# Kernel optimization log

Hardware: AMD Instinct MI355X
Metric: run time of the kernel (lower is better)

Reference implementation:

```python
import jax, jax.numpy as jnp
import numpy as np

N = 100000      # n_nodes
E = 1600000     # n_edges (avg degree 16)
F_IN = 128      # data.num_features
HID = 16        # hidden dim from ChebConv(F_IN, 16, K=2)
K = 2


def setup_inputs() -> dict:
    key = jax.random.key(0)
    k0, k1, k2, k3 = jax.random.split(key, 4)
    x = jax.random.normal(k0, (N, F_IN), dtype=jnp.float32)
    edge_index = jax.random.randint(k1, (2, E), 0, N, dtype=jnp.int64)
    W1 = jax.random.normal(k2, (K, F_IN, HID), dtype=jnp.float32) / np.float32(np.sqrt(F_IN))
    b1 = jnp.zeros((HID,), jnp.float32)
    W2 = jax.random.normal(k3, (K, HID, F_IN), dtype=jnp.float32) / np.float32(np.sqrt(HID))
    b2 = jnp.zeros((F_IN,), jnp.float32)
    return {"x": x, "edge_index": edge_index, "W1": W1, "b1": b1, "W2": W2, "b2": b2}


def _cheb_conv_k2(x, row, col, w_edge, W, b):
    # PyG ChebConv, K=2, sym norm, lambda_max=2:
    #   L_hat = 2L/lambda_max - I = -D^{-1/2} A D^{-1/2}
    #   out = Tx0 @ W[0] + Tx1 @ W[1] + b,  Tx0 = x, Tx1 = L_hat x
    Tx1 = jax.ops.segment_sum(x[col] * w_edge[:, None], row, num_segments=N)
    return x @ W[0] + Tx1 @ W[1] + b


def reference(x, edge_index, W1, b1, W2, b2):
    row, col = edge_index[0], edge_index[1]
    deg = jax.ops.segment_sum(jnp.ones((E,), x.dtype), row, num_segments=N)
    dinv = jnp.where(deg > 0, jax.lax.rsqrt(jnp.maximum(deg, 1.0)), 0.0)
    w_edge = -dinv[row] * dinv[col]  # scaled-Laplacian edge weights
    h = jax.nn.relu(_cheb_conv_k2(x, row, col, w_edge, W1, b1))
    # F.dropout(training=False) in eval -> identity
    out = _cheb_conv_k2(h, row, col, w_edge, W2, b2)
    return jax.nn.log_softmax(out, axis=1)
```

## Files before the change

kernel.cpp:

```cpp
#include <hip/hip_runtime.h>

#define N_NODES 100000
#define N_EDGES 1600000
#define NBKT 391
#define BCAP2 4608

__global__ __launch_bounds__(256) void binit_kernel(unsigned* __restrict__ bucketcur) {
    int b = blockIdx.x * 256 + threadIdx.x;
    if (b < NBKT) bucketcur[b] = (unsigned)b * BCAP2;
}

__global__ __launch_bounds__(256) void part_kernel(const int* __restrict__ row,
                                                   const int* __restrict__ col,
                                                   unsigned* __restrict__ bucketcur,
                                                   unsigned* __restrict__ entries, int E) {
    __shared__ unsigned h[NBKT];
    int t = threadIdx.x;
    for (int i = t; i < NBKT; i += 256) h[i] = 0;
    __syncthreads();
    int base_i = blockIdx.x * 4096;
    int r[16], c[16];
#pragma unroll
    for (int k = 0; k < 16; ++k) {
        int i = base_i + k * 256 + t;
        if (i < E) {
            r[k] = row[i]; c[k] = col[i];
            atomicAdd(&h[r[k] >> 8], 1u);
        } else r[k] = -1;
    }
    __syncthreads();
    for (int i = t; i < NBKT; i += 256) {
        unsigned cnt = h[i];
        if (cnt) h[i] = atomicAdd(&bucketcur[i], cnt);
    }
    __syncthreads();
#pragma unroll
    for (int k = 0; k < 16; ++k) {
        if (r[k] >= 0) {
            unsigned bkt = (unsigned)(r[k] >> 8);
            unsigned slot = atomicAdd(&h[bkt], 1u);
            if (slot < (bkt + 1u) * BCAP2)
                entries[slot] = ((unsigned)(r[k] & 255) << 24) | (unsigned)c[k];
        }
    }
}

__global__ __launch_bounds__(1024) void csr_kernel(const unsigned* __restrict__ bucketcur,
                                                   unsigned* __restrict__ entries,
                                                   uint2* __restrict__ rs_deg,
                                                   float* __restrict__ dinv, int n) {
    __shared__ unsigned se[BCAP2];
    __shared__ unsigned cnt[256];
    __shared__ unsigned sc[256];
    __shared__ unsigned cur[256];
    int t = threadIdx.x, b = blockIdx.x;
    if (t < 256) cnt[t] = 0;
    __syncthreads();
    unsigned base = (unsigned)b * BCAP2;
    unsigned m = bucketcur[b] - base;
    if (m > BCAP2) m = BCAP2;
    for (unsigned j = t; j < m; j += 1024) {
        unsigned e = entries[base + j];
        se[j] = e;
        atomicAdd(&cnt[e >> 24], 1u);
    }
    __syncthreads();
    if (t < 256) sc[t] = cnt[t];
    __syncthreads();
    for (int s = 1; s < 256; s <<= 1) {
        unsigned a = (t < 256 && t >= s) ? sc[t - s] : 0u;
        __syncthreads();
        if (t < 256) sc[t] += a;
        __syncthreads();
    }
    if (t < 256) {
        unsigned excl = sc[t] - cnt[t];
        cur[t] = excl;
        int node = b * 256 + t;
        if (node < n) {
            rs_deg[node] = make_uint2(base + excl, cnt[t]);
            dinv[node] = cnt[t] ? rsqrtf((float)cnt[t]) : 0.f;
        }
    }
    __syncthreads();
    for (unsigned j = t; j < m; j += 1024) {
        unsigned e = se[j];
        unsigned pos = atomicAdd(&cur[e >> 24], 1u);
        entries[base + pos] = e & 0xFFFFFF;
    }
}

__global__ __launch_bounds__(256) void proj1_kernel(const float* __restrict__ x,
                                                    const float* __restrict__ W1,
                                                    const float* __restrict__ dinv,
                                                    float* __restrict__ P0,
                                                    float* __restrict__ P1s, int n) {
    __shared__ float xs[64 * 132];
    __shared__ float wt[32 * 132];
    int t = threadIdx.x;
    int base = blockIdx.x * 64;
    for (int idx = t; idx < 32 * 128; idx += 256) {
        int j = idx >> 7, k = idx & 127;
        int r = (j & 7) * 4 + (j >> 3);
        wt[r * 132 + k] = W1[((j >> 4) ? 2048 : 0) + k * 16 + (j & 15)];
    }
    for (int idx = t; idx < 2048; idx += 256) {
        int row = idx >> 5, c4 = idx & 31;
        int node = base + row;
        float4 v = make_float4(0.f, 0.f, 0.f, 0.f);
        if (node < n) v = *(const float4*)&x[(size_t)node * 128 + c4 * 4];
        *(float4*)&xs[row * 132 + c4 * 4] = v;
    }
    __syncthreads();
    int nl = t >> 2, q = t & 3;
    int node = base + nl;
    float acc[8] = {0.f, 0.f, 0.f, 0.f, 0.f, 0.f, 0.f, 0.f};
    const float* xr = xs + nl * 132;
    const float* wb = wt + q * 132;
#pragma unroll 4
    for (int kb = 0; kb < 32; ++kb) {
        float4 xv = *(const float4*)&xr[kb * 4];
#pragma unroll
        for (int jj = 0; jj < 8; ++jj) {
            float4 wv = *(const float4*)&wb[jj * 4 * 132 + kb * 4];
            acc[jj] += xv.x * wv.x + xv.y * wv.y + xv.z * wv.z + xv.w * wv.w;
        }
    }
    if (node >= n) return;
    if (q < 2) {
        *(float4*)&P0[(size_t)node * 16 + q * 8]     = make_float4(acc[0], acc[1], acc[2], acc[3]);
        *(float4*)&P0[(size_t)node * 16 + q * 8 + 4] = make_float4(acc[4], acc[5], acc[6], acc[7]);
    } else {
        float dr = dinv[node];
        int o = (q - 2) * 8;
        *(float4*)&P1s[(size_t)node * 16 + o]     = make_float4(acc[0]*dr, acc[1]*dr, acc[2]*dr, acc[3]*dr);
        *(float4*)&P1s[(size_t)node * 16 + o + 4] = make_float4(acc[4]*dr, acc[5]*dr, acc[6]*dr, acc[7]*dr);
    }
}

__global__ __launch_bounds__(256) void agg1_kernel(const uint2* __restrict__ rs_deg,
                                                   const unsigned* __restrict__ ecol,
                                                   const float* __restrict__ dinv,
                                                   const float* __restrict__ P1s,
                                                   const float* __restrict__ b1,
                                                   float* __restrict__ H,
                                                   float* __restrict__ HS, int n) {
    int wave = threadIdx.x >> 6, lane = threadIdx.x & 63;
    int node = blockIdx.x * 4 + wave;
    if (node >= n) return;
    int fq = lane & 3, slot = lane >> 2;
    uint2 rd = rs_deg[node];
    float4 s4 = make_float4(0.f, 0.f, 0.f, 0.f);
    for (unsigned j = slot; j < rd.y; j += 16) {
        unsigned c = ecol[rd.x + j];
        float4 v = *(const float4*)&P1s[(size_t)c * 16 + fq * 4];
        s4.x += v.x; s4.y += v.y; s4.z += v.z; s4.w += v.w;
    }
#pragma unroll
    for (int st = 4; st < 64; st <<= 1) {
        s4.x += __shfl_xor(s4.x, st);
        s4.y += __shfl_xor(s4.y, st);
        s4.z += __shfl_xor(s4.z, st);
        s4.w += __shfl_xor(s4.w, st);
    }
    if (lane < 4) {
        float dr = dinv[node];
        float4 p  = *(float4*)&H[(size_t)node * 16 + lane * 4];
        float4 bb = *(const float4*)&b1[lane * 4];
        float4 v;
        v.x = fmaxf(p.x - dr * s4.x + bb.x, 0.f);
        v.y = fmaxf(p.y - dr * s4.y + bb.y, 0.f);
        v.z = fmaxf(p.z - dr * s4.z + bb.z, 0.f);
        v.w = fmaxf(p.w - dr * s4.w + bb.w, 0.f);
        *(float4*)&H[(size_t)node * 16 + lane * 4] = v;
        *(float4*)&HS[(size_t)node * 16 + lane * 4] =
            make_float4(v.x * dr, v.y * dr, v.z * dr, v.w * dr);
    }
}

__global__ __launch_bounds__(256) void agg2_kernel(const uint2* __restrict__ rs_deg,
                                                   const unsigned* __restrict__ ecol,
                                                   const float* __restrict__ dinv,
                                                   const float* __restrict__ HS,
                                                   float* __restrict__ T2, int n) {
    int wave = threadIdx.x >> 6, lane = threadIdx.x & 63;
    int node = blockIdx.x * 4 + wave;
    if (node >= n) return;
    int fq = lane & 3, slot = lane >> 2;
    uint2 rd = rs_deg[node];
    float4 s4 = make_float4(0.f, 0.f, 0.f, 0.f);
    for (unsigned j = slot; j < rd.y; j += 16) {
        unsigned c = ecol[rd.x + j];
        float4 v = *(const float4*)&HS[(size_t)c * 16 + fq * 4];
        s4.x += v.x; s4.y += v.y; s4.z += v.z; s4.w += v.w;
    }
#pragma unroll
    for (int st = 4; st < 64; st <<= 1) {
        s4.x += __shfl_xor(s4.x, st);
        s4.y += __shfl_xor(s4.y, st);
        s4.z += __shfl_xor(s4.z, st);
        s4.w += __shfl_xor(s4.w, st);
    }
    if (lane < 4) {
        float dr = -dinv[node];
        *(float4*)&T2[(size_t)node * 16 + lane * 4] =
            make_float4(dr * s4.x, dr * s4.y, dr * s4.z, dr * s4.w);
    }
}

__global__ __launch_bounds__(256) void out_gemm_kernel(const float* __restrict__ H,
                                                       const float* __restrict__ T2,
                                                       const float* __restrict__ W2,
                                                       const float* __restrict__ b2,
                                                       float* __restrict__ out, int n) {
    int wl = threadIdx.x >> 6, lane = threadIdx.x & 63;
    int nbase = blockIdx.x * 32 + wl * 8;

    float w00[16], w01[16], w10[16], w11[16];
#pragma unroll
    for (int k = 0; k < 16; ++k) {
        w00[k] = W2[k * 128 + lane];
        w01[k] = W2[2048 + k * 128 + lane];
        w10[k] = W2[k * 128 + lane + 64];
        w11[k] = W2[2048 + k * 128 + lane + 64];
    }
    float bb0 = b2[lane], bb1 = b2[lane + 64];

#pragma unroll 1
    for (int i = 0; i < 8; ++i) {
        int node = __builtin_amdgcn_readfirstlane(nbase + i);
        if (node >= n) return;
        const float* hp = H + (size_t)node * 16;
        const float* tp = T2 + (size_t)node * 16;
        float4 h0 = *(const float4*)&hp[0];
        float4 h1 = *(const float4*)&hp[4];
        float4 h2 = *(const float4*)&hp[8];
        float4 h3 = *(const float4*)&hp[12];
        float4 t0 = *(const float4*)&tp[0];
        float4 t1 = *(const float4*)&tp[4];
        float4 t2 = *(const float4*)&tp[8];
        float4 t3 = *(const float4*)&tp[12];
        float hv[16] = {h0.x,h0.y,h0.z,h0.w, h1.x,h1.y,h1.z,h1.w,
                        h2.x,h2.y,h2.z,h2.w, h3.x,h3.y,h3.z,h3.w};
        float tv[16] = {t0.x,t0.y,t0.z,t0.w, t1.x,t1.y,t1.z,t1.w,
                        t2.x,t2.y,t2.z,t2.w, t3.x,t3.y,t3.z,t3.w};
        float o0 = bb0, o1 = bb1;
#pragma unroll
        for (int k = 0; k < 16; ++k) {
            o0 += hv[k] * w00[k] + tv[k] * w01[k];
            o1 += hv[k] * w10[k] + tv[k] * w11[k];
        }
        float mx = fmaxf(o0, o1);
#pragma unroll
        for (int st = 1; st < 64; st <<= 1) mx = fmaxf(mx, __shfl_xor(mx, st));
        float ssum = expf(o0 - mx) + expf(o1 - mx);
#pragma unroll
        for (int st = 1; st < 64; st <<= 1) ssum += __shfl_xor(ssum, st);
        float lse = mx + logf(ssum);
        out[(size_t)node * 128 + lane]      = o0 - lse;
        out[(size_t)node * 128 + lane + 64] = o1 - lse;
    }
}

extern "C" void kernel_launch(void* const* d_in, const int* in_sizes, int n_in,
                              void* d_out, int out_size, void* d_ws, size_t ws_size,
                              hipStream_t stream) {
    const float* x  = (const float*)d_in[0];
    const int*   ei = (const int*)d_in[1];
    const float* W1 = (const float*)d_in[2];
    const float* b1 = (const float*)d_in[3];
    const float* W2 = (const float*)d_in[4];
    const float* b2 = (const float*)d_in[5];
    float* out = (float*)d_out;

    const int n = N_NODES, E = N_EDGES;
    const int* row = ei;
    const int* col = ei + E;

    const size_t NPAD = 100096;
    unsigned* bucketcur = (unsigned*)d_ws;
    uint2*    rs_deg    = (uint2*)(bucketcur + 512);
    float*    dinv      = (float*)(rs_deg + NPAD);
    unsigned* entries   = (unsigned*)(dinv + NPAD);
    float*    P0        = (float*)(entries + (size_t)NBKT * BCAP2);
    float*    P1s       = P0 + NPAD * 16;
    float*    HS        = P1s + NPAD * 16;
    float*    T2        = P1s;

    binit_kernel<<<2, 256, 0, stream>>>(bucketcur);
    part_kernel<<<NBKT, 256, 0, stream>>>(row, col, bucketcur, entries, E);
    csr_kernel<<<NBKT, 1024, 0, stream>>>(bucketcur, entries, rs_deg, dinv, n);
    proj1_kernel<<<(n + 63) / 64, 256, 0, stream>>>(x, W1, dinv, P0, P1s, n);
    agg1_kernel<<<(n + 3) / 4, 256, 0, stream>>>(rs_deg, entries, dinv, P1s, b1, P0, HS, n);
    agg2_kernel<<<(n + 3) / 4, 256, 0, stream>>>(rs_deg, entries, dinv, HS, T2, n);
    out_gemm_kernel<<<(n + 31) / 32, 256, 0, stream>>>(P0, T2, W2, b2, out, n);
}
```

Before: 184.2 us.

## Rewrite proj1 as one-thread-per-node GEMV with weights read via uniform loads

Replaces the shared-memory tiled projection (64 nodes per block, 4 threads per node) with a scheme where each thread computes all 32 outputs for one node. It streams the node's x row directly from global memory with a one-step prefetch and reads W1 with wave-uniform addresses, so those loads can go through scalar/constant caching. This removes the LDS staging and the barrier, but each thread reads a 512-byte row with strided per-lane access, which coalesces poorly, and it holds 32 accumulators in registers. The grid is changed to NBKT blocks of 256 threads, which covers the node count.

```diff
diff --git a/kernel.cpp b/kernel.cpp
--- a/kernel.cpp
+++ b/kernel.cpp
@@ -95,46 +95,41 @@
                                                     const float* __restrict__ dinv,
                                                     float* __restrict__ P0,
                                                     float* __restrict__ P1s, int n) {
-    __shared__ float xs[64 * 132];
-    __shared__ float wt[32 * 132];
-    int t = threadIdx.x;
-    int base = blockIdx.x * 64;
-    for (int idx = t; idx < 32 * 128; idx += 256) {
-        int j = idx >> 7, k = idx & 127;
-        int r = (j & 7) * 4 + (j >> 3);
-        wt[r * 132 + k] = W1[((j >> 4) ? 2048 : 0) + k * 16 + (j & 15)];
-    }
-    for (int idx = t; idx < 2048; idx += 256) {
-        int row = idx >> 5, c4 = idx & 31;
-        int node = base + row;
-        float4 v = make_float4(0.f, 0.f, 0.f, 0.f);
-        if (node < n) v = *(const float4*)&x[(size_t)node * 128 + c4 * 4];
-        *(float4*)&xs[row * 132 + c4 * 4] = v;
-    }
-    __syncthreads();
-    int nl = t >> 2, q = t & 3;
-    int node = base + nl;
-    float acc[8] = {0.f, 0.f, 0.f, 0.f, 0.f, 0.f, 0.f, 0.f};
-    const float* xr = xs + nl * 132;
-    const float* wb = wt + q * 132;
-#pragma unroll 4
+    int node = blockIdx.x * 256 + threadIdx.x;
+    bool valid = node < n;
+    const float* xr = x + (valid ? (size_t)node * 128 : 0);
+
+    float acc0[16], acc1[16];
+#pragma unroll
+    for (int j = 0; j < 16; ++j) { acc0[j] = 0.f; acc1[j] = 0.f; }
+
+    float4 xv = *(const float4*)xr;
+#pragma unroll 2
     for (int kb = 0; kb < 32; ++kb) {
-        float4 xv = *(const float4*)&xr[kb * 4];
-#pragma unroll
-        for (int jj = 0; jj < 8; ++jj) {
-            float4 wv = *(const float4*)&wb[jj * 4 * 132 + kb * 4];
-            acc[jj] += xv.x * wv.x + xv.y * wv.y + xv.z * wv.z + xv.w * wv.w;
-        }
-    }
-    if (node >= n) return;
-    if (q < 2) {
-        *(float4*)&P0[(size_t)node * 16 + q * 8]     = make_float4(acc[0], acc[1], acc[2], acc[3]);
-        *(float4*)&P0[(size_t)node * 16 + q * 8 + 4] = make_float4(acc[4], acc[5], acc[6], acc[7]);
-    } else {
-        float dr = dinv[node];
-        int o = (q - 2) * 8;
-        *(float4*)&P1s[(size_t)node * 16 + o]     = make_float4(acc[0]*dr, acc[1]*dr, acc[2]*dr, acc[3]*dr);
-        *(float4*)&P1s[(size_t)node * 16 + o + 4] = make_float4(acc[4]*dr, acc[5]*dr, acc[6]*dr, acc[7]*dr);
+        float4 xn = make_float4(0.f, 0.f, 0.f, 0.f);
+        if (kb < 31) xn = *(const float4*)&xr[(kb + 1) * 4];
+        const float* w0 = W1 + kb * 64;
+        const float* w1 = W1 + 2048 + kb * 64;
+        float xk[4] = {xv.x, xv.y, xv.z, xv.w};
+#pragma unroll
+        for (int kk = 0; kk < 4; ++kk) {
+#pragma unroll
+            for (int j = 0; j < 16; ++j) {
+                acc0[j] += xk[kk] * w0[kk * 16 + j];
+                acc1[j] += xk[kk] * w1[kk * 16 + j];
+            }
+        }
+        xv = xn;
+    }
+
+    if (!valid) return;
+    float dr = dinv[node];
+#pragma unroll
+    for (int jq = 0; jq < 4; ++jq) {
+        *(float4*)&P0[(size_t)node * 16 + jq * 4] =
+            make_float4(acc0[jq*4+0], acc0[jq*4+1], acc0[jq*4+2], acc0[jq*4+3]);
+        *(float4*)&P1s[(size_t)node * 16 + jq * 4] =
+            make_float4(acc1[jq*4+0]*dr, acc1[jq*4+1]*dr, acc1[jq*4+2]*dr, acc1[jq*4+3]*dr);
     }
 }
 
@@ -290,7 +285,7 @@
     binit_kernel<<<2, 256, 0, stream>>>(bucketcur);
     part_kernel<<<NBKT, 256, 0, stream>>>(row, col, bucketcur, entries, E);
     csr_kernel<<<NBKT, 1024, 0, stream>>>(bucketcur, entries, rs_deg, dinv, n);
-    proj1_kernel<<<(n + 63) / 64, 256, 0, stream>>>(x, W1, dinv, P0, P1s, n);
+    proj1_kernel<<<NBKT, 256, 0, stream>>>(x, W1, dinv, P0, P1s, n);
     agg1_kernel<<<(n + 3) / 4, 256, 0, stream>>>(rs_deg, entries, dinv, P1s, b1, P0, HS, n);
     agg2_kernel<<<(n + 3) / 4, 256, 0, stream>>>(rs_deg, entries, dinv, HS, T2, n);
     out_gemm_kernel<<<(n + 31) / 32, 256, 0, stream>>>(P0, T2, W2, b2, out, n);
```

New measurement: 183.6 us. No clear change (-0.3%).
